# Kernel optimization log

Measured on AMD Instinct MI355X. Metric: run time of the kernel, lower is better.

Reference implementation:

```python
import jax, jax.numpy as jnp
import numpy as np

N_MEL = 80; ENC = 512; ARNN = 1024; DRNN = 1024; PRE = 256
ADIM = 128; NFILT = 32; KS = 31
B = 16; T_ENC = 128; T_DEC = 128
NEG = -1e30  # stand-in for -inf mask value


def _lstm_cell(x, h, c, wih, whh, bih, bhh):
    # PyTorch LSTMCell gate order: i, f, g, o
    gates = x @ wih.T + h @ whh.T + bih + bhh
    i, f, g, o = jnp.split(gates, 4, axis=-1)
    c = jax.nn.sigmoid(f) * c + jax.nn.sigmoid(i) * jnp.tanh(g)
    h = jax.nn.sigmoid(o) * jnp.tanh(c)
    return h, c


def _forward(memory, mels, memory_lengths, prenet_w1, prenet_w2,
             arnn_wih, arnn_whh, arnn_bih, arnn_bhh,
             query_w, memory_w, v_w, loc_conv_w, loc_dense_w,
             drnn_wih, drnn_whh, drnn_bih, drnn_bhh,
             proj_w, proj_b, gate_w, gate_b):
    bsz, t_enc, enc = memory.shape
    t_dec = mels.shape[2]
    valid = jnp.arange(t_enc)[None, :] < memory_lengths[:, None]  # [B,T_enc]
    proc_mem = memory @ memory_w.T  # [B,T_enc,ADIM], precomputed once

    # parse_decoder_inputs + go frame: use go frame + teacher frames 0..T-2
    teacher = jnp.transpose(mels, (2, 0, 1))  # [T_dec,B,n_mel]
    go = jnp.zeros((1, bsz, mels.shape[1]), mels.dtype)
    dec_in = jnp.concatenate([go, teacher], axis=0)[:t_dec]
    # Prenet (dropout is p=0.0 in source, so omitted)
    x = jax.nn.relu(dec_in @ prenet_w1.T)
    x = jax.nn.relu(x @ prenet_w2.T)  # [T_dec,B,PRE]

    pad = (KS - 1) // 2

    def step(carry, x_t):
        attn_h, attn_c, dec_h, dec_c, aw, awc, ctx = carry
        # attention RNN
        cell_in = jnp.concatenate([x_t, ctx], axis=-1)
        attn_h2, attn_c2 = _lstm_cell(cell_in, attn_h, attn_c,
                                      arnn_wih, arnn_whh, arnn_bih, arnn_bhh)
        # location-sensitive attention
        aw_cat = jnp.stack([aw, awc], axis=1)  # [B,2,T_enc]
        loc = jax.lax.conv_general_dilated(
            aw_cat, loc_conv_w, (1,), [(pad, pad)],
            dimension_numbers=('NCH', 'OIH', 'NCH'))  # [B,NFILT,T_enc]
        loc = jnp.einsum('bft,af->bta', loc, loc_dense_w)  # [B,T_enc,ADIM]
        pq = attn_h2 @ query_w.T  # [B,ADIM]
        e = jnp.tanh(pq[:, None, :] + loc + proc_mem) @ v_w[0]  # [B,T_enc]
        e = jnp.where(valid, e, NEG)
        aw2 = jax.nn.softmax(e, axis=1)
        ctx2 = jnp.einsum('bt,bte->be', aw2, memory)  # [B,ENC]
        awc2 = awc + aw2
        # decoder RNN
        dec_in2 = jnp.concatenate([attn_h2, ctx2], axis=-1)
        dec_h2, dec_c2 = _lstm_cell(dec_in2, dec_h, dec_c,
                                    drnn_wih, drnn_whh, drnn_bih, drnn_bhh)
        hc = jnp.concatenate([dec_h2, ctx2], axis=-1)
        mel = hc @ proj_w.T + proj_b      # [B,n_mel]
        gate = hc @ gate_w.T + gate_b     # [B,1]
        new_carry = (attn_h2, attn_c2, dec_h2, dec_c2, aw2, awc2, ctx2)
        return new_carry, (mel, gate[:, 0], aw2)

    z = lambda *s: jnp.zeros(s, memory.dtype)
    carry0 = (z(bsz, ARNN), z(bsz, ARNN), z(bsz, DRNN), z(bsz, DRNN),
              z(bsz, t_enc), z(bsz, t_enc), z(bsz, enc))
    _, (mels_out, gates, aligns) = jax.lax.scan(step, carry0, x)
    mel_outputs = jnp.transpose(mels_out, (1, 2, 0))   # [B,n_mel,T_dec]
    gate_outputs = jnp.transpose(gates, (1, 0))        # [B,T_dec]
    alignments = jnp.transpose(aligns, (1, 0, 2))      # [B,T_dec,T_enc]
    return mel_outputs, gate_outputs, alignments


def setup_inputs() -> dict:
    key = jax.random.key(0)
    ks = jax.random.split(key, 24)

    def g(i, shape):
        fan_in = shape[-1] if len(shape) <= 2 else int(np.prod(shape[1:]))
        return jax.random.normal(ks[i], shape, jnp.float32) / np.float32(np.sqrt(fan_in))

    return {
        'memory': jax.random.normal(ks[0], (B, T_ENC, ENC), jnp.float32),
        'mels': jax.random.normal(ks[1], (B, N_MEL, T_DEC), jnp.float32),
        'memory_lengths': jax.random.randint(ks[2], (B,), T_ENC // 2, T_ENC + 1),
        'prenet_w1': g(3, (PRE, N_MEL)),
        'prenet_w2': g(4, (PRE, PRE)),
        'arnn_wih': g(5, (4 * ARNN, PRE + ENC)),
        'arnn_whh': g(6, (4 * ARNN, ARNN)),
        'arnn_bih': g(7, (4 * ARNN,)),
        'arnn_bhh': g(8, (4 * ARNN,)),
        'query_w': g(9, (ADIM, ARNN)),
        'memory_w': g(10, (ADIM, ENC)),
        'v_w': g(11, (1, ADIM)),
        'loc_conv_w': g(12, (NFILT, 2, KS)),
        'loc_dense_w': g(13, (ADIM, NFILT)),
        'drnn_wih': g(14, (4 * DRNN, ARNN + ENC)),
        'drnn_whh': g(15, (4 * DRNN, DRNN)),
        'drnn_bih': g(16, (4 * DRNN,)),
        'drnn_bhh': g(17, (4 * DRNN,)),
        'proj_w': g(18, (N_MEL, DRNN + ENC)),
        'proj_b': g(19, (N_MEL,)),
        'gate_w': g(20, (1, DRNN + ENC)),
        'gate_b': g(21, (1,)),
    }


def reference(memory, mels, memory_lengths, prenet_w1, prenet_w2,
              arnn_wih, arnn_whh, arnn_bih, arnn_bhh,
              query_w, memory_w, v_w, loc_conv_w, loc_dense_w,
              drnn_wih, drnn_whh, drnn_bih, drnn_bhh,
              proj_w, proj_b, gate_w, gate_b):
    return _forward(memory, mels, memory_lengths, prenet_w1, prenet_w2,
                    arnn_wih, arnn_whh, arnn_bih, arnn_bhh,
                    query_w, memory_w, v_w, loc_conv_w, loc_dense_w,
                    drnn_wih, drnn_whh, drnn_bih, drnn_bhh,
                    proj_w, proj_b, gate_w, gate_b)
```

## Files before the change

kernel.cpp:

```cpp
#include <hip/hip_runtime.h>
#include <hip/hip_cooperative_groups.h>

namespace cg = cooperative_groups;

#define N_MEL 80
#define ENC   512
#define ARNN  1024
#define PRE   256
#define ADIM  128
#define NFILT 32
#define KS    31
#define BSZ   16
#define TENC  128
#define TDEC  128

#define OFF_XA     0u
#define OFF_X      8388608u
#define OFF_H1     8912896u
#define OFF_DECIN  9437184u
#define OFF_PM     9601024u
#define OFF_ATTNH  9863168u
#define OFF_DECH   9895936u
#define OFF_CTX    9928704u
#define OFF_CTR    9945088u
#define STATE_FLOATS 82496

typedef float vf4 __attribute__((ext_vector_type(4)));

__device__ __forceinline__ float sigmf(float x) { return 1.0f / (1.0f + __expf(-x)); }
__device__ __forceinline__ float tanhfast(float x) { return 1.0f - 2.0f / (__expf(2.0f * x) + 1.0f); }
__device__ __forceinline__ float dot4(const float4& w, const vf4& x) {
    return w.x * x.x + w.y * x.y + w.z * x.z + w.w * x.w;
}
__device__ __forceinline__ float dot4f(const float4& w, const float4& x) {
    return w.x * x.x + w.y * x.y + w.z * x.z + w.w * x.w;
}

__device__ __forceinline__ vf4 vload4(const float* p) { return *(const volatile vf4*)p; }
__device__ __forceinline__ float vloadf(const float* p) { return *(const volatile float*)p; }
__device__ __forceinline__ void vstoref(float* p, float v) { *(volatile float*)p = v; }

__device__ __forceinline__ void wait_ge(unsigned* p, unsigned tgt) {
    while (__hip_atomic_load(p, __ATOMIC_RELAXED, __HIP_MEMORY_SCOPE_AGENT) < tgt)
        __builtin_amdgcn_s_sleep(1);
    asm volatile("" ::: "memory");
}


__global__ void __launch_bounds__(1024) build_decin(const float* __restrict__ mels,
                                                    float* __restrict__ decin) {
    int idx = blockIdx.x * 1024 + threadIdx.x;
    if (idx >= 128 * 16 * 80) return;
    int t = idx / 1280, r = idx % 1280;
    int b = r / 80, m = r % 80;
    decin[idx] = (t == 0) ? 0.f : mels[b * (80 * 128) + m * 128 + (t - 1)];
}

__global__ void __launch_bounds__(256) gemm_kernel(
    const float* __restrict__ A, int lda,
    const float* __restrict__ B, int ldb,
    float* __restrict__ C, int ldc,
    int M, int N, int K,
    const float* __restrict__ bias1, const float* __restrict__ bias2, int relu) {
    __shared__ float As[16][68];
    __shared__ float Bs[16][68];
    int tid = threadIdx.x;
    int tn = tid & 15, tm = tid >> 4;
    int m0 = blockIdx.y * 64, n0 = blockIdx.x * 64;
    float acc[4][4] = {};
    for (int k0 = 0; k0 < K; k0 += 16) {
        for (int idx = tid; idx < 1024; idx += 256) {
            int mm = idx >> 4, kk = idx & 15;
            int kg = k0 + kk;
            As[kk][mm] = (kg < K) ? A[(size_t)(m0 + mm) * lda + kg] : 0.f;
            Bs[kk][mm] = (kg < K) ? B[(size_t)(n0 + mm) * ldb + kg] : 0.f;
        }
        __syncthreads();
#pragma unroll
        for (int kk = 0; kk < 16; kk++) {
            float av[4], bv[4];
#pragma unroll
            for (int i = 0; i < 4; i++) { av[i] = As[kk][tm * 4 + i]; bv[i] = Bs[kk][tn * 4 + i]; }
#pragma unroll
            for (int i = 0; i < 4; i++)
#pragma unroll
                for (int j = 0; j < 4; j++) acc[i][j] += av[i] * bv[j];
        }
        __syncthreads();
    }
    for (int i = 0; i < 4; i++) {
        int m = m0 + tm * 4 + i;
        for (int j = 0; j < 4; j++) {
            int n = n0 + tn * 4 + j;
            float v = acc[i][j];
            if (bias1) v += bias1[n];
            if (bias2) v += bias2[n];
            if (relu) v = fmaxf(v, 0.f);
            C[(size_t)m * ldc + n] = v;
        }
    }
}


struct DecArgs {
    const float* memory;
    const int* memlen;
    const float* arnn_wih;
    const float* arnn_whh;
    const float* drnn_wih;
    const float* drnn_whh;
    const float* drnn_bih;
    const float* drnn_bhh;
    const float* query_w;
    const float* v_w;
    const float* conv_w;
    const float* dense_w;
    const float* proj_w;
    const float* proj_b;
    const float* gate_w;
    const float* gate_b;
    float* ws;
    float* out;
};

__global__ void __launch_bounds__(512, 2) decoder_main(DecArgs A) {
    cg::grid_group grid = cg::this_grid();
    const int tid = threadIdx.x;
    const int wv = tid >> 6;
    const int l = tid & 63;
    const int blk = blockIdx.x;
    const int u = wv & 3;
    const int kq = wv >> 2;
    const int jj = blk * 4 + u;
    const int col = kq * 256 + l * 4;
    float* ws = A.ws;
    unsigned* ctrA = (unsigned*)(ws + OFF_CTR);
    unsigned* ctrB = (unsigned*)(ws + OFF_CTR + 32);
    const int grp = blk >> 4;
    unsigned* subA = (unsigned*)(ws + OFF_CTR + 64 + grp * 32);

    __shared__ float s_pm[128 * 132];
    __shared__ float s_loc[128 * 33];
    __shared__ float s_dw[128 * 33];
    __shared__ float s_cw[1984];
    __shared__ float s_ah[1024];
    __shared__ float s_ep[512];
    __shared__ float s_part[8][64];
    __shared__ float s_pq[128];
    __shared__ float s_ev[128];
    __shared__ float s_aw2[128];
    __shared__ float s_awl[128];
    __shared__ float s_awcl[128];
    __shared__ float s_attnc[64];
    __shared__ float s_decc[64];
    __shared__ float s_db[16];
    __shared__ float s_vw[128];
    __shared__ float s_red[2];

    {
        int g = blk * 512 + tid;
        if (g < STATE_FLOATS) ws[OFF_ATTNH + g] = 0.f;
    }
    if (tid < 128) { s_awl[tid] = 0.f; s_awcl[tid] = 0.f; }
    if (tid < 64) { s_attnc[tid] = 0.f; s_decc[tid] = 0.f; }
    if (tid < 16) {
        int uu = tid >> 2, gg = tid & 3;
        s_db[tid] = A.drnn_bih[gg * 1024 + blk * 4 + uu] + A.drnn_bhh[gg * 1024 + blk * 4 + uu];
    }
    if (tid < 128) s_vw[tid] = A.v_w[tid];
    for (int idx = tid; idx < 4096; idx += 512) {
        int a = idx >> 5, f = idx & 31;
        s_dw[a * 33 + f] = A.dense_w[idx];
    }
    if (blk < 16) {
        for (int idx = tid; idx < 16384; idx += 512) {
            int tt = idx >> 7, a = idx & 127;
            s_pm[tt * 132 + a] = ws[OFF_PM + (blk * 128 + tt) * 128 + a];
        }
        for (int idx = tid; idx < 1984; idx += 512) s_cw[idx] = A.conv_w[idx];
    }
    const int ml = (blk < 16) ? A.memlen[blk] : 0;

    float4 wA[12];
    {
#pragma unroll
        for (int g = 0; g < 4; g++)
            wA[g] = *reinterpret_cast<const float4*>(
                A.arnn_wih + (size_t)(g * 1024 + jj) * 768 + 256 + col);
#pragma unroll
        for (int ch = 1; ch < 3; ch++)
#pragma unroll
            for (int g = 0; g < 4; g++)
                wA[ch * 4 + g] = *reinterpret_cast<const float4*>(
                    A.arnn_whh + (size_t)(g * 1024 + jj) * 1024 + (ch - 1) * 512 + col);
    }
    float4 wD[20];
    {
#pragma unroll
        for (int ch = 0; ch < 3; ch++)
#pragma unroll
            for (int g = 0; g < 4; g++)
                wD[ch * 4 + g] = *reinterpret_cast<const float4*>(
                    A.drnn_wih + (size_t)(g * 1024 + jj) * 1536 + ch * 512 + col);
#pragma unroll
        for (int ch = 3; ch < 5; ch++)
#pragma unroll
            for (int g = 0; g < 4; g++)
                wD[ch * 4 + g] = *reinterpret_cast<const float4*>(
                    A.drnn_whh + (size_t)(g * 1024 + jj) * 1024 + (ch - 3) * 512 + col);
    }
    __syncthreads();
    grid.sync();

    auto reduce4 = [&](float p0, float p1, float p2, float p3) -> float {
        float a01 = (l & 1) ? p1 : p0;
        float b01 = (l & 1) ? p0 : p1;
        a01 += __shfl_xor(b01, 1);
        float a23 = (l & 1) ? p3 : p2;
        float b23 = (l & 1) ? p2 : p3;
        a23 += __shfl_xor(b23, 1);
        float k_ = (l & 2) ? a23 : a01;
        float s_ = (l & 2) ? a01 : a23;
        k_ += __shfl_xor(s_, 2);
        k_ += __shfl_xor(k_, 4);
        k_ += __shfl_xor(k_, 8);
        k_ += __shfl_xor(k_, 16);
        k_ += __shfl_xor(k_, 32);
        return k_;
    };

    auto attn_stage = [&](int t, int wpar, int rpar) {
        const float* hb = ws + OFF_ATTNH + rpar * 16384;
        const float* cb = ws + OFF_CTX + rpar * 8192;
        float xa0 = 0.f, xa1 = 0.f, xa2 = 0.f, xa3 = 0.f;
        if (tid < 64) {
            int eb = tid & 15, eu = tid >> 4;
            const float* xa = ws + OFF_XA + (size_t)(t * 16 + eb) * 4096 + (blk * 4 + eu);
            xa0 = xa[0]; xa1 = xa[1024]; xa2 = xa[2048]; xa3 = xa[3072];
        }
#pragma unroll 4
        for (int b = 0; b < 16; b++) {
            vf4 x0 = vload4(cb + b * 512 + col);
            vf4 x1 = vload4(hb + b * 1024 + col);
            vf4 x2 = vload4(hb + b * 1024 + 512 + col);
            float p0 = dot4(wA[0], x0) + dot4(wA[4], x1) + dot4(wA[8], x2);
            float p1 = dot4(wA[1], x0) + dot4(wA[5], x1) + dot4(wA[9], x2);
            float p2 = dot4(wA[2], x0) + dot4(wA[6], x1) + dot4(wA[10], x2);
            float p3 = dot4(wA[3], x0) + dot4(wA[7], x1) + dot4(wA[11], x2);
            float r = reduce4(p0, p1, p2, p3);
            if (l < 4) s_part[wv][b * 4 + l] = r;
        }
        __syncthreads();
        if (tid < 64) {
            int eu = tid >> 4, eb = tid & 15;
            float G0 = s_part[eu][eb * 4 + 0] + s_part[eu + 4][eb * 4 + 0] + xa0;
            float G1 = s_part[eu][eb * 4 + 1] + s_part[eu + 4][eb * 4 + 1] + xa1;
            float G2 = s_part[eu][eb * 4 + 2] + s_part[eu + 4][eb * 4 + 2] + xa2;
            float G3 = s_part[eu][eb * 4 + 3] + s_part[eu + 4][eb * 4 + 3] + xa3;
            float ig = sigmf(G0), fg = sigmf(G1), gg = tanhfast(G2), og = sigmf(G3);
            float c = fg * s_attnc[tid] + ig * gg;
            s_attnc[tid] = c;
            vstoref(ws + OFF_ATTNH + wpar * 16384 + eb * 1024 + blk * 4 + eu, og * tanhfast(c));
        }
    };

    auto dec_stage = [&](int wpar, int rpar) {
        const float* hb = ws + OFF_ATTNH + wpar * 16384;
        const float* cb = ws + OFF_CTX + wpar * 8192;
        const float* db = ws + OFF_DECH + rpar * 16384;
#pragma unroll 2
        for (int b = 0; b < 16; b++) {
            vf4 x0 = vload4(hb + b * 1024 + col);
            vf4 x1 = vload4(hb + b * 1024 + 512 + col);
            vf4 x2 = vload4(cb + b * 512 + col);
            vf4 x3 = vload4(db + b * 1024 + col);
            vf4 x4 = vload4(db + b * 1024 + 512 + col);
            float p0 = dot4(wD[0], x0) + dot4(wD[4], x1) + dot4(wD[8], x2) + dot4(wD[12], x3) + dot4(wD[16], x4);
            float p1 = dot4(wD[1], x0) + dot4(wD[5], x1) + dot4(wD[9], x2) + dot4(wD[13], x3) + dot4(wD[17], x4);
            float p2 = dot4(wD[2], x0) + dot4(wD[6], x1) + dot4(wD[10], x2) + dot4(wD[14], x3) + dot4(wD[18], x4);
            float p3 = dot4(wD[3], x0) + dot4(wD[7], x1) + dot4(wD[11], x2) + dot4(wD[15], x3) + dot4(wD[19], x4);
            float r = reduce4(p0, p1, p2, p3);
            if (l < 4) s_part[wv][b * 4 + l] = r;
        }
        __syncthreads();
        if (tid < 64) {
            int eu = tid >> 4, eb = tid & 15;
            float G0 = s_part[eu][eb * 4 + 0] + s_part[eu + 4][eb * 4 + 0] + s_db[eu * 4 + 0];
            float G1 = s_part[eu][eb * 4 + 1] + s_part[eu + 4][eb * 4 + 1] + s_db[eu * 4 + 1];
            float G2 = s_part[eu][eb * 4 + 2] + s_part[eu + 4][eb * 4 + 2] + s_db[eu * 4 + 2];
            float G3 = s_part[eu][eb * 4 + 3] + s_part[eu + 4][eb * 4 + 3] + s_db[eu * 4 + 3];
            float ig = sigmf(G0), fg = sigmf(G1), gg = tanhfast(G2), og = sigmf(G3);
            float c = fg * s_decc[tid] + ig * gg;
            s_decc[tid] = c;
            vstoref(ws + OFF_DECH + wpar * 16384 + eb * 1024 + blk * 4 + eu, og * tanhfast(c));
        }
        __syncthreads();
    };

    auto attention = [&](int t, int wpar) {
        const int b = blk;
        s_ah[tid] = vloadf(ws + OFF_ATTNH + wpar * 16384 + b * 1024 + tid);
        s_ah[tid + 512] = vloadf(ws + OFF_ATTNH + wpar * 16384 + b * 1024 + 512 + tid);
        __syncthreads();
        for (int idx = tid; idx < 4096; idx += 512) {
            int f = idx >> 7, tt = idx & 127;
            const float* w0 = s_cw + f * 62;
            float s = 0.f;
#pragma unroll
            for (int k = 0; k < 31; k++) {
                int j = tt + k - 15;
                if (j >= 0 && j < 128) s += w0[k] * s_awl[j] + w0[31 + k] * s_awcl[j];
            }
            s_loc[tt * 33 + f] = s;
        }
#pragma unroll 2
        for (int ii = 0; ii < 16; ii++) {
            int a = wv * 16 + ii;
            const float* qw = A.query_w + a * 1024;
            float s = 0.f;
#pragma unroll
            for (int q = 0; q < 4; q++) {
                int k = q * 256 + l * 4;
                float4 h4 = *reinterpret_cast<const float4*>(&s_ah[k]);
                float4 w4 = *reinterpret_cast<const float4*>(&qw[k]);
                s += dot4f(w4, h4);
            }
#pragma unroll
            for (int off = 1; off < 64; off <<= 1) s += __shfl_xor(s, off);
            if (l == 0) s_pq[a] = s;
        }
        __syncthreads();
        {
            int tt = tid >> 2, sl = tid & 3;
            float part = 0.f;
            for (int i = 0; i < 32; i++) {
                int a = i * 4 + sl;
                float lp = 0.f;
#pragma unroll
                for (int f = 0; f < 32; f++) lp += s_loc[tt * 33 + f] * s_dw[a * 33 + f];
                float arg = s_pq[a] + lp + s_pm[tt * 132 + a];
                part += s_vw[a] * tanhfast(arg);
            }
            s_ep[tid] = part;
        }
        __syncthreads();
        if (tid < 128) {
            float s = s_ep[tid * 4] + s_ep[tid * 4 + 1] + s_ep[tid * 4 + 2] + s_ep[tid * 4 + 3];
            if (tid >= ml) s = -1e30f;
            s_ev[tid] = s;
        }
        __syncthreads();
        if (wv == 0) {
            float m = fmaxf(s_ev[l], s_ev[l + 64]);
#pragma unroll
            for (int off = 1; off < 64; off <<= 1) m = fmaxf(m, __shfl_xor(m, off));
            if (l == 0) s_red[0] = m;
        }
        __syncthreads();
        if (tid < 128) s_aw2[tid] = __expf(s_ev[tid] - s_red[0]);
        __syncthreads();
        if (wv == 0) {
            float s = s_aw2[l] + s_aw2[l + 64];
#pragma unroll
            for (int off = 1; off < 64; off <<= 1) s += __shfl_xor(s, off);
            if (l == 0) s_red[1] = 1.f / s;
        }
        __syncthreads();
        if (tid < 128) {
            float val = s_aw2[tid] * s_red[1];
            s_aw2[tid] = val;
            s_awl[tid] = val;
            s_awcl[tid] += val;
            A.out[165888 + b * 16384 + t * 128 + tid] = val;
        }
        __syncthreads();
        {
            const float* mb = A.memory + (size_t)b * 65536 + tid;
            float acc = 0.f;
#pragma unroll 8
            for (int tt2 = 0; tt2 < 128; tt2++) acc += s_aw2[tt2] * mb[tt2 * 512];
            vstoref(ws + OFF_CTX + wpar * 8192 + b * 512 + tid, acc);
        }
    };

    auto eout = [&](int tdone) {
        int widx = (blk - 16) * 8 + wv;
        if (widx >= 1296) return;
        int ppar = tdone & 1;
        int b; const float* wrow; float bias; float* dst;
        if (widx < 1280) {
            b = widx / 80; int m = widx % 80;
            wrow = A.proj_w + m * 1536; bias = A.proj_b[m];
            dst = A.out + (size_t)(b * 80 + m) * 128 + tdone;
        } else {
            b = widx - 1280;
            wrow = A.gate_w; bias = A.gate_b[0];
            dst = A.out + 163840 + b * 128 + tdone;
        }
        const float* h1p = ws + OFF_DECH + ppar * 16384 + b * 1024;
        const float* c1p = ws + OFF_CTX + ppar * 8192 + b * 512;
        float s = 0.f;
#pragma unroll
        for (int q = 0; q < 6; q++) {
            int k = q * 256 + l * 4;
            float4 w4 = *reinterpret_cast<const float4*>(&wrow[k]);
            vf4 h4;
            if (k < 1024) h4 = vload4(h1p + k);
            else h4 = vload4(c1p + k - 1024);
            s += dot4(w4, h4);
        }
#pragma unroll
        for (int off = 1; off < 64; off <<= 1) s += __shfl_xor(s, off);
        if (l == 0) *dst = s + bias;
    };

    for (int t = 0; t < 128; t++) {
        int wpar = t & 1, rpar = wpar ^ 1;
        attn_stage(t, wpar, rpar);
        __syncthreads();
        if (tid == 0) {
            asm volatile("s_waitcnt vmcnt(0)" ::: "memory");
            unsigned old = __hip_atomic_fetch_add(subA, 1u, __ATOMIC_RELAXED,
                                                  __HIP_MEMORY_SCOPE_AGENT);
            if (old == 16u * (unsigned)(t + 1) - 1u)
                __hip_atomic_fetch_add(ctrA, 1u, __ATOMIC_RELAXED,
                                       __HIP_MEMORY_SCOPE_AGENT);
        }
        if (blk < 16) {
            if (tid == 0) wait_ge(ctrA, 16u * (unsigned)(t + 1));
            __syncthreads();
            attention(t, wpar);
            __syncthreads();
            if (tid == 0) {
                asm volatile("s_waitcnt vmcnt(0)" ::: "memory");
                __hip_atomic_fetch_add(ctrB, 1u, __ATOMIC_RELAXED,
                                       __HIP_MEMORY_SCOPE_AGENT);
                wait_ge(ctrB, 16u * (unsigned)(t + 1));
            }
            __syncthreads();
        } else {
            if (tid == 0) wait_ge(ctrA, 16u * (unsigned)(t + 1));
            __syncthreads();
            if (t >= 1) eout(t - 1);
            if (tid == 0) wait_ge(ctrB, 16u * (unsigned)(t + 1));
            __syncthreads();
        }
        dec_stage(wpar, rpar);
    }
    if (tid == 0) {
        asm volatile("s_waitcnt vmcnt(0)" ::: "memory");
        unsigned old = __hip_atomic_fetch_add(subA, 1u, __ATOMIC_RELAXED,
                                              __HIP_MEMORY_SCOPE_AGENT);
        if (old == 16u * 129u - 1u)
            __hip_atomic_fetch_add(ctrA, 1u, __ATOMIC_RELAXED, __HIP_MEMORY_SCOPE_AGENT);
    }
    if (blk >= 16) {
        if (tid == 0) wait_ge(ctrA, 16u * 129u);
        __syncthreads();
        eout(127);
    }
}


extern "C" void kernel_launch(void* const* d_in, const int* in_sizes, int n_in,
                              void* d_out, int out_size, void* d_ws, size_t ws_size,
                              hipStream_t stream) {
    (void)in_sizes; (void)n_in; (void)out_size; (void)ws_size;
    const float* memory    = (const float*)d_in[0];
    const float* mels      = (const float*)d_in[1];
    const int*   memlen    = (const int*)d_in[2];
    const float* prenet_w1 = (const float*)d_in[3];
    const float* prenet_w2 = (const float*)d_in[4];
    const float* arnn_wih  = (const float*)d_in[5];
    const float* arnn_whh  = (const float*)d_in[6];
    const float* arnn_bih  = (const float*)d_in[7];
    const float* arnn_bhh  = (const float*)d_in[8];
    const float* query_w   = (const float*)d_in[9];
    const float* memory_w  = (const float*)d_in[10];
    const float* v_w       = (const float*)d_in[11];
    const float* conv_w    = (const float*)d_in[12];
    const float* dense_w   = (const float*)d_in[13];
    const float* drnn_wih  = (const float*)d_in[14];
    const float* drnn_whh  = (const float*)d_in[15];
    const float* drnn_bih  = (const float*)d_in[16];
    const float* drnn_bhh  = (const float*)d_in[17];
    const float* proj_w    = (const float*)d_in[18];
    const float* proj_b    = (const float*)d_in[19];
    const float* gate_w    = (const float*)d_in[20];
    const float* gate_b    = (const float*)d_in[21];
    float* ws = (float*)d_ws;
    float* out = (float*)d_out;

    build_decin<<<dim3(160), dim3(1024), 0, stream>>>(mels, ws + OFF_DECIN);
    gemm_kernel<<<dim3(4, 32), dim3(256), 0, stream>>>(ws + OFF_DECIN, 80, prenet_w1, 80,
                                                       ws + OFF_H1, 256, 2048, 256, 80,
                                                       nullptr, nullptr, 1);
    gemm_kernel<<<dim3(4, 32), dim3(256), 0, stream>>>(ws + OFF_H1, 256, prenet_w2, 256,
                                                       ws + OFF_X, 256, 2048, 256, 256,
                                                       nullptr, nullptr, 1);
    gemm_kernel<<<dim3(64, 32), dim3(256), 0, stream>>>(ws + OFF_X, 256, arnn_wih, 768,
                                                        ws + OFF_XA, 4096, 2048, 4096, 256,
                                                        arnn_bih, arnn_bhh, 0);
    gemm_kernel<<<dim3(2, 32), dim3(256), 0, stream>>>(memory, 512, memory_w, 512,
                                                       ws + OFF_PM, 128, 2048, 128, 512,
                                                       nullptr, nullptr, 0);

    DecArgs a;
    a.memory = memory; a.memlen = memlen;
    a.arnn_wih = arnn_wih; a.arnn_whh = arnn_whh;
    a.drnn_wih = drnn_wih; a.drnn_whh = drnn_whh;
    a.drnn_bih = drnn_bih; a.drnn_bhh = drnn_bhh;
    a.query_w = query_w; a.v_w = v_w;
    a.conv_w = conv_w; a.dense_w = dense_w;
    a.proj_w = proj_w; a.proj_b = proj_b;
    a.gate_w = gate_w; a.gate_b = gate_b;
    a.ws = ws; a.out = out;
    void* kargs[] = { &a };
    hipLaunchCooperativeKernel((const void*)decoder_main, dim3(256), dim3(512),
                               kargs, 0, stream);
}
```

Baseline: 12.63 ms.

## Overlap context-independent decoder LSTM matvec with attention barrier wait

```diff
diff --git a/kernel.cpp b/kernel.cpp
--- a/kernel.cpp
+++ b/kernel.cpp
@@ -146,8 +146,8 @@
     __shared__ float s_ah[1024];
     __shared__ float s_ep[512];
     __shared__ float s_part[8][64];
+    __shared__ float s_pp[8][64];
     __shared__ float s_pq[128];
-    __shared__ float s_ev[128];
     __shared__ float s_aw2[128];
     __shared__ float s_awl[128];
     __shared__ float s_awcl[128];
@@ -264,31 +264,47 @@
         }
     };
 
-    auto dec_stage = [&](int wpar, int rpar) {
+    auto dec_partial = [&](int wpar, int rpar) {
         const float* hb = ws + OFF_ATTNH + wpar * 16384;
-        const float* cb = ws + OFF_CTX + wpar * 8192;
         const float* db = ws + OFF_DECH + rpar * 16384;
 #pragma unroll 2
         for (int b = 0; b < 16; b++) {
             vf4 x0 = vload4(hb + b * 1024 + col);
             vf4 x1 = vload4(hb + b * 1024 + 512 + col);
-            vf4 x2 = vload4(cb + b * 512 + col);
             vf4 x3 = vload4(db + b * 1024 + col);
             vf4 x4 = vload4(db + b * 1024 + 512 + col);
-            float p0 = dot4(wD[0], x0) + dot4(wD[4], x1) + dot4(wD[8], x2) + dot4(wD[12], x3) + dot4(wD[16], x4);
-            float p1 = dot4(wD[1], x0) + dot4(wD[5], x1) + dot4(wD[9], x2) + dot4(wD[13], x3) + dot4(wD[17], x4);
-            float p2 = dot4(wD[2], x0) + dot4(wD[6], x1) + dot4(wD[10], x2) + dot4(wD[14], x3) + dot4(wD[18], x4);
-            float p3 = dot4(wD[3], x0) + dot4(wD[7], x1) + dot4(wD[11], x2) + dot4(wD[15], x3) + dot4(wD[19], x4);
+            float p0 = dot4(wD[0], x0) + dot4(wD[4], x1) + dot4(wD[12], x3) + dot4(wD[16], x4);
+            float p1 = dot4(wD[1], x0) + dot4(wD[5], x1) + dot4(wD[13], x3) + dot4(wD[17], x4);
+            float p2 = dot4(wD[2], x0) + dot4(wD[6], x1) + dot4(wD[14], x3) + dot4(wD[18], x4);
+            float p3 = dot4(wD[3], x0) + dot4(wD[7], x1) + dot4(wD[15], x3) + dot4(wD[19], x4);
+            float r = reduce4(p0, p1, p2, p3);
+            if (l < 4) s_pp[wv][b * 4 + l] = r;
+        }
+    };
+
+    auto dec_tail = [&](int wpar) {
+        const float* cb = ws + OFF_CTX + wpar * 8192;
+#pragma unroll 4
+        for (int b = 0; b < 16; b++) {
+            vf4 x2 = vload4(cb + b * 512 + col);
+            float p0 = dot4(wD[8], x2);
+            float p1 = dot4(wD[9], x2);
+            float p2 = dot4(wD[10], x2);
+            float p3 = dot4(wD[11], x2);
             float r = reduce4(p0, p1, p2, p3);
             if (l < 4) s_part[wv][b * 4 + l] = r;
         }
         __syncthreads();
         if (tid < 64) {
             int eu = tid >> 4, eb = tid & 15;
-            float G0 = s_part[eu][eb * 4 + 0] + s_part[eu + 4][eb * 4 + 0] + s_db[eu * 4 + 0];
-            float G1 = s_part[eu][eb * 4 + 1] + s_part[eu + 4][eb * 4 + 1] + s_db[eu * 4 + 1];
-            float G2 = s_part[eu][eb * 4 + 2] + s_part[eu + 4][eb * 4 + 2] + s_db[eu * 4 + 2];
-            float G3 = s_part[eu][eb * 4 + 3] + s_part[eu + 4][eb * 4 + 3] + s_db[eu * 4 + 3];
+            float G0 = s_part[eu][eb * 4 + 0] + s_part[eu + 4][eb * 4 + 0]
+                     + s_pp[eu][eb * 4 + 0] + s_pp[eu + 4][eb * 4 + 0] + s_db[eu * 4 + 0];
+            float G1 = s_part[eu][eb * 4 + 1] + s_part[eu + 4][eb * 4 + 1]
+                     + s_pp[eu][eb * 4 + 1] + s_pp[eu + 4][eb * 4 + 1] + s_db[eu * 4 + 1];
+            float G2 = s_part[eu][eb * 4 + 2] + s_part[eu + 4][eb * 4 + 2]
+                     + s_pp[eu][eb * 4 + 2] + s_pp[eu + 4][eb * 4 + 2] + s_db[eu * 4 + 2];
+            float G3 = s_part[eu][eb * 4 + 3] + s_part[eu + 4][eb * 4 + 3]
+                     + s_pp[eu][eb * 4 + 3] + s_pp[eu + 4][eb * 4 + 3] + s_db[eu * 4 + 3];
             float ig = sigmf(G0), fg = sigmf(G1), gg = tanhfast(G2), og = sigmf(G3);
             float c = fg * s_decc[tid] + ig * gg;
             s_decc[tid] = c;
@@ -301,7 +317,6 @@
         const int b = blk;
         s_ah[tid] = vloadf(ws + OFF_ATTNH + wpar * 16384 + b * 1024 + tid);
         s_ah[tid + 512] = vloadf(ws + OFF_ATTNH + wpar * 16384 + b * 1024 + 512 + tid);
-        __syncthreads();
         for (int idx = tid; idx < 4096; idx += 512) {
             int f = idx >> 7, tt = idx & 127;
             const float* w0 = s_cw + f * 62;
@@ -313,7 +328,8 @@
             }
             s_loc[tt * 33 + f] = s;
         }
-#pragma unroll 2
+        __syncthreads();
+#pragma unroll 4
         for (int ii = 0; ii < 16; ii++) {
             int a = wv * 16 + ii;
             const float* qw = A.query_w + a * 1024;
@@ -346,28 +362,18 @@
         __syncthreads();
         if (tid < 128) {
             float s = s_ep[tid * 4] + s_ep[tid * 4 + 1] + s_ep[tid * 4 + 2] + s_ep[tid * 4 + 3];
-            if (tid >= ml) s = -1e30f;
-            s_ev[tid] = s;
-        }
-        __syncthreads();
-        if (wv == 0) {
-            float m = fmaxf(s_ev[l], s_ev[l + 64]);
-#pragma unroll
-            for (int off = 1; off < 64; off <<= 1) m = fmaxf(m, __shfl_xor(m, off));
-            if (l == 0) s_red[0] = m;
-        }
-        __syncthreads();
-        if (tid < 128) s_aw2[tid] = __expf(s_ev[tid] - s_red[0]);
+            s_aw2[tid] = (tid >= ml) ? 0.f : __expf(s);
+        }
         __syncthreads();
         if (wv == 0) {
             float s = s_aw2[l] + s_aw2[l + 64];
 #pragma unroll
             for (int off = 1; off < 64; off <<= 1) s += __shfl_xor(s, off);
-            if (l == 0) s_red[1] = 1.f / s;
+            if (l == 0) s_red[0] = 1.f / s;
         }
         __syncthreads();
         if (tid < 128) {
-            float val = s_aw2[tid] * s_red[1];
+            float val = s_aw2[tid] * s_red[0];
             s_aw2[tid] = val;
             s_awl[tid] = val;
             s_awcl[tid] += val;
@@ -435,17 +441,20 @@
                 asm volatile("s_waitcnt vmcnt(0)" ::: "memory");
                 __hip_atomic_fetch_add(ctrB, 1u, __ATOMIC_RELAXED,
                                        __HIP_MEMORY_SCOPE_AGENT);
-                wait_ge(ctrB, 16u * (unsigned)(t + 1));
             }
+            dec_partial(wpar, rpar);
+            if (tid == 0) wait_ge(ctrB, 16u * (unsigned)(t + 1));
             __syncthreads();
+            dec_tail(wpar);
         } else {
             if (tid == 0) wait_ge(ctrA, 16u * (unsigned)(t + 1));
             __syncthreads();
             if (t >= 1) eout(t - 1);
+            dec_partial(wpar, rpar);
             if (tid == 0) wait_ge(ctrB, 16u * (unsigned)(t + 1));
             __syncthreads();
-        }
-        dec_stage(wpar, rpar);
+            dec_tail(wpar);
+        }
     }
     if (tid == 0) {
         asm volatile("s_waitcnt vmcnt(0)" ::: "memory");
```

Result: faster. 12.00 ms (-5.0%).
